# Kernel tuning notes

Hardware: AMD Instinct MI355X
Metric: run time of the kernel (lower is better)

## Reference

```python
import jax, jax.numpy as jnp
import numpy as np

B, T, C = 4, 2048, 768
H = 12  # n_head; head_dim = C // H = 64


def setup_inputs() -> dict:
    key = jax.random.key(0)
    k1, k2, k3, k4, k5 = jax.random.split(key, 5)
    scale = 0.02
    return {
        "x": jax.random.normal(k1, (B, T, C), dtype=jnp.float32),
        "w_attn": jax.random.normal(k2, (C, 3 * C), dtype=jnp.float32) * scale,
        "b_attn": jax.random.normal(k3, (3 * C,), dtype=jnp.float32) * scale,
        "w_proj": jax.random.normal(k4, (C, C), dtype=jnp.float32) * scale,
        "b_proj": jax.random.normal(k5, (C,), dtype=jnp.float32) * scale,
    }


def reference(x, w_attn, b_attn, w_proj, b_proj):
    Bx, Tx, Cx = x.shape
    hd = Cx // H  # head dim
    qkv = x @ w_attn + b_attn                       # [B, T, 3C]
    q, k, v = jnp.split(qkv, 3, axis=2)
    # [B, T, H, hd] -> [B, H, T, hd]
    q = q.reshape(Bx, Tx, H, hd).transpose(0, 2, 1, 3)
    k = k.reshape(Bx, Tx, H, hd).transpose(0, 2, 1, 3)
    v = v.reshape(Bx, Tx, H, hd).transpose(0, 2, 1, 3)
    att = jnp.einsum('bhqd,bhkd->bhqk', q, k) / jnp.sqrt(jnp.float32(hd))
    causal = jnp.tril(jnp.ones((Tx, Tx), dtype=bool))
    att = jnp.where(causal[None, None, :, :], att, -jnp.inf)
    att = jax.nn.softmax(att, axis=-1)
    y = jnp.einsum('bhqk,bhkd->bhqd', att, v)       # [B, H, T, hd]
    y = y.transpose(0, 2, 1, 3).reshape(Bx, Tx, Cx)
    return y @ w_proj + b_proj
```

## Files before the change

kernel.cpp:

```cpp
#include <hip/hip_runtime.h>
#include <hip/hip_bf16.h>

using f32x4 = __attribute__((ext_vector_type(4))) float;
using s16x8 = __attribute__((ext_vector_type(8))) short;

#define MFMA16x16x32(a, b, c) __builtin_amdgcn_mfma_f32_16x16x32_bf16((a), (b), (c), 0, 0, 0)

#define AS_G(p) ((const __attribute__((address_space(1))) void*)(p))
#define AS_L(p) ((__attribute__((address_space(3))) void*)(p))

#define BARRIER_LGKM() do { \
    asm volatile("s_waitcnt lgkmcnt(0)" ::: "memory"); \
    __builtin_amdgcn_s_barrier(); \
} while (0)

static __device__ __forceinline__ unsigned short f2bf(float f) {
    unsigned int u = __float_as_uint(f);
    u = (u + 0x7fffu + ((u >> 16) & 1u)) >> 16;
    return (unsigned short)u;
}
static __device__ __forceinline__ unsigned int cvt_pk_bf2(float lo, float hi) {
    unsigned int r;
    asm("v_cvt_pk_bf16_f32 %0, %1, %2" : "=v"(r) : "v"(lo), "v"(hi));
    return r;
}
static __device__ __forceinline__ int swz128(int r, int c) { return (r * 128 + c) ^ ((r & 7) << 4); }

__global__ __launch_bounds__(256)
void prologue_kernel(const float* __restrict__ x, unsigned short* __restrict__ xb,
                     const float* __restrict__ w_attn, unsigned short* __restrict__ wTa,
                     const float* __restrict__ w_proj, unsigned short* __restrict__ wTp) {
    __shared__ float tile[32][33];
    const int bid = blockIdx.x, tid = threadIdx.x;
    if (bid < 2048) {
        const int n = 8192 * 768;
        int i = (bid * 256 + tid) * 4;
        const int stride = 2048 * 256 * 4;
        for (; i < n; i += stride) {
            float4 v = *(const float4*)(x + i);
            ushort4 o;
            o.x = f2bf(v.x); o.y = f2bf(v.y); o.z = f2bf(v.z); o.w = f2bf(v.w);
            *(ushort4*)(xb + i) = o;
        }
    } else {
        const float* w; unsigned short* wt; int K, N, bx, by;
        if (bid < 3776) {
            int id = bid - 2048; w = w_attn; wt = wTa; K = 768; N = 2304;
            bx = id % 72; by = id / 72;
        } else {
            int id = bid - 3776; w = w_proj; wt = wTp; K = 768; N = 768;
            bx = id % 24; by = id / 24;
        }
        const int tx = tid & 31, ty = tid >> 5;
        const int n0 = bx * 32, k0 = by * 32;
#pragma unroll
        for (int r = 0; r < 4; r++)
            tile[ty * 4 + r][tx] = w[(size_t)(k0 + ty * 4 + r) * N + n0 + tx];
        __syncthreads();
#pragma unroll
        for (int r = 0; r < 4; r++)
            wt[(size_t)(n0 + ty * 4 + r) * K + k0 + tx] = f2bf(tile[tx][ty * 4 + r]);
    }
}

template <bool OUT_BF16>
__global__ __launch_bounds__(256, 2)
void gemm_bt(const unsigned short* __restrict__ A, const unsigned short* __restrict__ Bt,
             const float* __restrict__ bias, void* __restrict__ Cout,
             unsigned short* __restrict__ Vt,
             int M, int N, int K, int ldc, int qcols, float qscale) {
    __shared__ char smem[65536];
    const int tid = threadIdx.x, wid = tid >> 6, lane = tid & 63;
    const int g = lane >> 4, lr = lane & 15;
    const int m0 = blockIdx.y * 128, n0 = blockIdx.x * 128;
    const int wm = wid >> 1, wn = wid & 1;

    f32x4 acc[4][4];
#pragma unroll
    for (int i = 0; i < 4; i++)
#pragma unroll
        for (int j = 0; j < 4; j++) acc[i][j] = f32x4{0.f, 0.f, 0.f, 0.f};

    const int rbase = lane >> 3;
    const int cSw = ((lane & 7) << 4) ^ (rbase << 4);

    auto STAGE = [&](int buf, int kt) {
        char* base = smem + buf * 32768;
#pragma unroll
        for (int ww = 0; ww < 4; ww++) {
            int w = wid * 4 + ww;
            int r = w * 8 + rbase;
            const unsigned short* srcA = A + (size_t)(m0 + r) * K + kt + (cSw >> 1);
            __builtin_amdgcn_global_load_lds(AS_G(srcA), AS_L(base + w * 1024), 16, 0, 0);
            const unsigned short* srcB = Bt + (size_t)(n0 + r) * K + kt + (cSw >> 1);
            __builtin_amdgcn_global_load_lds(AS_G(srcB), AS_L(base + 16384 + w * 1024), 16, 0, 0);
        }
    };

    const int nk = K >> 6;
    STAGE(0, 0);

    for (int t = 0; t < nk; t++) {
        if (t + 1 < nk) {
            STAGE((t + 1) & 1, (t + 1) << 6);
            asm volatile("s_waitcnt vmcnt(8)" ::: "memory");
        } else {
            asm volatile("s_waitcnt vmcnt(0)" ::: "memory");
        }
        __builtin_amdgcn_s_barrier();
        char* cbase = smem + (t & 1) * 32768;
#pragma unroll
        for (int ks = 0; ks < 2; ks++) {
            s16x8 af[4], bfr[4];
#pragma unroll
            for (int i = 0; i < 4; i++)
                af[i] = *(const s16x8*)(cbase + swz128(wm * 64 + i * 16 + lr, ks * 64 + g * 16));
#pragma unroll
            for (int j = 0; j < 4; j++)
                bfr[j] = *(const s16x8*)(cbase + 16384 + swz128(wn * 64 + j * 16 + lr, ks * 64 + g * 16));
#pragma unroll
            for (int i = 0; i < 4; i++)
#pragma unroll
                for (int j = 0; j < 4; j++)
                    acc[i][j] = MFMA16x16x32(af[i], bfr[j], acc[i][j]);
        }
        BARRIER_LGKM();
    }

#pragma unroll
    for (int j = 0; j < 4; j++) {
        int c = n0 + wn * 64 + j * 16 + lr;
        float bv = bias[c];
        float cscale = (c < qcols) ? qscale : 1.0f;
        if (Vt != nullptr && c >= 1536) {
            int h = (c - 1536) >> 6, d = (c - 1536) & 63;
#pragma unroll
            for (int i = 0; i < 4; i++) {
                int r0 = m0 + wm * 64 + i * 16 + g * 4;
                int bb = r0 >> 11, t0 = r0 & 2047;
                ushort4 o4;
                o4.x = f2bf(acc[i][j][0] + bv);
                o4.y = f2bf(acc[i][j][1] + bv);
                o4.z = f2bf(acc[i][j][2] + bv);
                o4.w = f2bf(acc[i][j][3] + bv);
                *(ushort4*)(Vt + ((((size_t)bb * 12 + h) * 64 + d) << 11) + t0) = o4;
            }
        } else {
#pragma unroll
            for (int i = 0; i < 4; i++) {
#pragma unroll
                for (int rg = 0; rg < 4; rg++) {
                    int r = m0 + wm * 64 + i * 16 + g * 4 + rg;
                    float val = (acc[i][j][rg] + bv) * cscale;
                    if constexpr (OUT_BF16)
                        ((unsigned short*)Cout)[(size_t)r * ldc + c] = f2bf(val);
                    else
                        ((float*)Cout)[(size_t)r * ldc + c] = val;
                }
            }
        }
    }
}

__global__ __launch_bounds__(256, 2)
void attn_kernel(const unsigned short* __restrict__ qk, const unsigned short* __restrict__ Vt,
                 unsigned short* __restrict__ y) {
    __shared__ char smem[40960];
    const int tid = threadIdx.x, wid = tid >> 6, lane = tid & 63;
    const int g = lane >> 4, lr = lane & 15;
    const int T = 2048;

    const int s = blockIdx.x;
    const int xcd = s & 7, i = s >> 3;
    const int grp = xcd * 6 + (i >> 4);
    const int qpi = i & 15;
    const int h = grp % 12, b = grp / 12;
    const int qtA = qpi, qtB = 31 - qpi;
    const int q0A = qtA * 64, q0B = qtB * 64;

    const int krow = tid >> 2;
    const int kcol = (tid & 3) * 32;

    const unsigned short* qrowA = qk + (size_t)(b * T + q0A + wid * 16 + lr) * 1536 + h * 64;
    const unsigned short* qrowB = qk + (size_t)(b * T + q0B + wid * 16 + lr) * 1536 + h * 64;
    s16x8 aqA[2], aqB[2];
    aqA[0] = *(const s16x8*)(qrowA + g * 8);
    aqA[1] = *(const s16x8*)(qrowA + 32 + g * 8);
    aqB[0] = *(const s16x8*)(qrowB + g * 8);
    aqB[1] = *(const s16x8*)(qrowB + 32 + g * 8);

    float lA = 0.f, lB = 0.f;
    f32x4 oA[4], oB[4];
#pragma unroll
    for (int r = 0; r < 4; r++) { oA[r] = f32x4{0.f, 0.f, 0.f, 0.f}; oB[r] = f32x4{0.f, 0.f, 0.f, 0.f}; }

    const unsigned short* pkBase = qk + (size_t)(b * T + krow) * 1536 + 768 + h * 64 + (kcol >> 1);
    const unsigned short* pvBase = Vt + ((((size_t)b * 12 + h) * 64 + krow) << 11) + (kcol >> 1);

    const int ntA = qtA + 1, ntB = qtB + 1;

    s16x8 k0 = *(const s16x8*)(pkBase);
    s16x8 k1 = *(const s16x8*)(pkBase + 8);
    s16x8 v0 = *(const s16x8*)(pvBase);
    s16x8 v1 = *(const s16x8*)(pvBase + 8);
    *(s16x8*)(smem + swz128(krow, kcol)) = k0;
    *(s16x8*)(smem + swz128(krow, kcol + 16)) = k1;
    *(s16x8*)(smem + 16384 + swz128(krow, kcol)) = v0;
    *(s16x8*)(smem + 16384 + swz128(krow, kcol + 16)) = v1;
    if (ntB > 1) {
        const unsigned short* pk = pkBase + (size_t)64 * 1536;
        k0 = *(const s16x8*)(pk);
        k1 = *(const s16x8*)(pk + 8);
        const unsigned short* pv = pvBase + 64;
        v0 = *(const s16x8*)(pv);
        v1 = *(const s16x8*)(pv + 8);
    }
    BARRIER_LGKM();

    char* const pbase = smem + 32768 + wid * 2048;
    const int q_rel = wid * 16 + lr;

    for (int t = 0; t < ntB; t++) {
        char* kbase = smem + (t & 1) * 8192;
        char* vbase = smem + 16384 + (t & 1) * 8192;

        {
            f32x4 st[4];
            __builtin_amdgcn_s_setprio(1);
#pragma unroll
            for (int nf = 0; nf < 4; nf++) {
                f32x4 sf = f32x4{0.f, 0.f, 0.f, 0.f};
#pragma unroll
                for (int ks = 0; ks < 2; ks++) {
                    s16x8 ak = *(const s16x8*)(kbase + swz128(nf * 16 + lr, (ks * 32 + g * 8) * 2));
                    sf = MFMA16x16x32(ak, aqB[ks], sf);
                }
                st[nf] = sf;
            }
            __builtin_amdgcn_s_setprio(0);

            const bool diag = (t == ntB - 1);
#pragma unroll
            for (int nf = 0; nf < 4; nf++)
#pragma unroll
                for (int rg = 0; rg < 4; rg++) {
                    float p = exp2f(st[nf][rg]);
                    if (diag && (nf * 16 + g * 4 + rg > q_rel)) p = 0.f;
                    st[nf][rg] = p;
                    lB += p;
                }

#pragma unroll
            for (int nf = 0; nf < 4; nf++) {
                uint2 dw;
                dw.x = cvt_pk_bf2(st[nf][0], st[nf][1]);
                dw.y = cvt_pk_bf2(st[nf][2], st[nf][3]);
                *(uint2*)(pbase + swz128(lr, nf * 32 + g * 8)) = dw;
            }
            s16x8 pf[2];
#pragma unroll
            for (int ks = 0; ks < 2; ks++)
                pf[ks] = *(const s16x8*)(pbase + swz128(lr, ks * 64 + g * 16));

            __builtin_amdgcn_s_setprio(1);
#pragma unroll
            for (int nf = 0; nf < 4; nf++) {
#pragma unroll
                for (int ks = 0; ks < 2; ks++) {
                    s16x8 bv = *(const s16x8*)(vbase + swz128(nf * 16 + lr, ks * 64 + g * 16));
                    oB[nf] = MFMA16x16x32(pf[ks], bv, oB[nf]);
                }
            }
            __builtin_amdgcn_s_setprio(0);
        }

        if (t < ntA) {
            f32x4 st[4];
            __builtin_amdgcn_s_setprio(1);
#pragma unroll
            for (int nf = 0; nf < 4; nf++) {
                f32x4 sf = f32x4{0.f, 0.f, 0.f, 0.f};
#pragma unroll
                for (int ks = 0; ks < 2; ks++) {
                    s16x8 ak = *(const s16x8*)(kbase + swz128(nf * 16 + lr, (ks * 32 + g * 8) * 2));
                    sf = MFMA16x16x32(ak, aqA[ks], sf);
                }
                st[nf] = sf;
            }
            __builtin_amdgcn_s_setprio(0);

            const bool diag = (t == ntA - 1);
#pragma unroll
            for (int nf = 0; nf < 4; nf++)
#pragma unroll
                for (int rg = 0; rg < 4; rg++) {
                    float p = exp2f(st[nf][rg]);
                    if (diag && (nf * 16 + g * 4 + rg > q_rel)) p = 0.f;
                    st[nf][rg] = p;
                    lA += p;
                }

#pragma unroll
            for (int nf = 0; nf < 4; nf++) {
                uint2 dw;
                dw.x = cvt_pk_bf2(st[nf][0], st[nf][1]);
                dw.y = cvt_pk_bf2(st[nf][2], st[nf][3]);
                *(uint2*)(pbase + swz128(lr, nf * 32 + g * 8)) = dw;
            }
            s16x8 pf[2];
#pragma unroll
            for (int ks = 0; ks < 2; ks++)
                pf[ks] = *(const s16x8*)(pbase + swz128(lr, ks * 64 + g * 16));

            __builtin_amdgcn_s_setprio(1);
#pragma unroll
            for (int nf = 0; nf < 4; nf++) {
#pragma unroll
                for (int ks = 0; ks < 2; ks++) {
                    s16x8 bv = *(const s16x8*)(vbase + swz128(nf * 16 + lr, ks * 64 + g * 16));
                    oA[nf] = MFMA16x16x32(pf[ks], bv, oA[nf]);
                }
            }
            __builtin_amdgcn_s_setprio(0);
        }

        if (t + 1 < ntB) {
            char* kn = smem + ((t + 1) & 1) * 8192;
            char* vn = smem + 16384 + ((t + 1) & 1) * 8192;
            *(s16x8*)(kn + swz128(krow, kcol)) = k0;
            *(s16x8*)(kn + swz128(krow, kcol + 16)) = k1;
            *(s16x8*)(vn + swz128(krow, kcol)) = v0;
            *(s16x8*)(vn + swz128(krow, kcol + 16)) = v1;
            if (t + 2 < ntB) {
                const unsigned short* pk = pkBase + (size_t)(t + 2) * 64 * 1536;
                k0 = *(const s16x8*)(pk);
                k1 = *(const s16x8*)(pk + 8);
                const unsigned short* pv = pvBase + (t + 2) * 64;
                v0 = *(const s16x8*)(pv);
                v1 = *(const s16x8*)(pv + 8);
            }
        }
        BARRIER_LGKM();
    }

#pragma unroll
    for (int which = 0; which < 2; which++) {
        float l = which ? lB : lA;
        l += __shfl_xor(l, 16, 64);
        l += __shfl_xor(l, 32, 64);
        float linv = 1.0f / l;
        float linv_q[4];
#pragma unroll
        for (int rg = 0; rg < 4; rg++)
            linv_q[rg] = __shfl(linv, (lane & 48) | (g * 4 + rg), 64);
        const int q0 = which ? q0B : q0A;
        f32x4* o = which ? oB : oA;
#pragma unroll
        for (int nf = 0; nf < 4; nf++) {
#pragma unroll
            for (int rg = 0; rg < 4; rg++) {
                int row = b * T + q0 + wid * 16 + g * 4 + rg;
                int col = h * 64 + nf * 16 + lr;
                y[(size_t)row * 768 + col] = f2bf(o[nf][rg] * linv_q[rg]);
            }
        }
    }
}

extern "C" void kernel_launch(void* const* d_in, const int* in_sizes, int n_in,
                              void* d_out, int out_size, void* d_ws, size_t ws_size,
                              hipStream_t stream) {
    const float* x      = (const float*)d_in[0];
    const float* w_attn = (const float*)d_in[1];
    const float* b_attn = (const float*)d_in[2];
    const float* w_proj = (const float*)d_in[3];
    const float* b_proj = (const float*)d_in[4];

    char* ws = (char*)d_ws;
    unsigned short* qk  = (unsigned short*)(ws);
    unsigned short* Vt  = (unsigned short*)(ws + 25165824);
    unsigned short* wTa = (unsigned short*)(ws + 37748736);
    unsigned short* wTp = (unsigned short*)(ws + 41287680);

    const bool big = ws_size >= (size_t)55050240;
    unsigned short* xb = (unsigned short*)d_out;
    unsigned short* yb = big ? (unsigned short*)(ws + 42467328)
                             : (unsigned short*)((char*)d_out + 12582912);
    float* projOut = big ? (float*)d_out : (float*)ws;

    prologue_kernel<<<4352, 256, 0, stream>>>(x, xb, w_attn, wTa, w_proj, wTp);

    gemm_bt<true><<<dim3(18, 64), 256, 0, stream>>>(xb, wTa, b_attn, (void*)qk, Vt,
                                                    8192, 2304, 768, 1536, 768, 0.1803368801111244f);
    attn_kernel<<<768, 256, 0, stream>>>(qk, Vt, yb);
    gemm_bt<false><<<dim3(6, 64), 256, 0, stream>>>(yb, wTp, b_proj, (void*)projOut, nullptr,
                                                    8192, 768, 768, 768, 0, 1.0f);
    if (!big)
        hipMemcpyAsync(d_out, projOut, 25165824, hipMemcpyDeviceToDevice, stream);
}
```

Baseline: 132.2 us.

## Interleave two query tiles' softmax stages and compute row sums via MFMA

Gives the A and B query tiles separate P buffers in LDS so both score/exp phases run before both PV phases, letting the two independent chains overlap. The per-lane scalar row-sum accumulation and the final shuffles are replaced by MFMAs of P against a vector of bf16 ones. exp2f is swapped for the hardware exp2 builtin. In exchange, LDS use rises to 48 KB, which may affect occupancy, and the row sums are now taken over bf16-rounded P values.

```diff
diff --git a/kernel.cpp b/kernel.cpp
--- a/kernel.cpp
+++ b/kernel.cpp
@@ -165,7 +165,7 @@
 __global__ __launch_bounds__(256, 2)
 void attn_kernel(const unsigned short* __restrict__ qk, const unsigned short* __restrict__ Vt,
                  unsigned short* __restrict__ y) {
-    __shared__ char smem[40960];
+    __shared__ char smem[49152];
     const int tid = threadIdx.x, wid = tid >> 6, lane = tid & 63;
     const int g = lane >> 4, lr = lane & 15;
     const int T = 2048;
@@ -181,6 +181,10 @@
     const int krow = tid >> 2;
     const int kcol = (tid & 3) * 32;
 
+    s16x8 vone;
+#pragma unroll
+    for (int e = 0; e < 8; e++) vone[e] = (short)0x3F80;
+
     const unsigned short* qrowA = qk + (size_t)(b * T + q0A + wid * 16 + lr) * 1536 + h * 64;
     const unsigned short* qrowB = qk + (size_t)(b * T + q0B + wid * 16 + lr) * 1536 + h * 64;
     s16x8 aqA[2], aqB[2];
@@ -189,10 +193,11 @@
     aqB[0] = *(const s16x8*)(qrowB + g * 8);
     aqB[1] = *(const s16x8*)(qrowB + 32 + g * 8);
 
-    float lA = 0.f, lB = 0.f;
-    f32x4 oA[4], oB[4];
+    f32x4 oA[4], oB[4], lsumA, lsumB;
 #pragma unroll
     for (int r = 0; r < 4; r++) { oA[r] = f32x4{0.f, 0.f, 0.f, 0.f}; oB[r] = f32x4{0.f, 0.f, 0.f, 0.f}; }
+    lsumA = f32x4{0.f, 0.f, 0.f, 0.f};
+    lsumB = f32x4{0.f, 0.f, 0.f, 0.f};
 
     const unsigned short* pkBase = qk + (size_t)(b * T + krow) * 1536 + 768 + h * 64 + (kcol >> 1);
     const unsigned short* pvBase = Vt + ((((size_t)b * 12 + h) * 64 + krow) << 11) + (kcol >> 1);
@@ -217,12 +222,14 @@
     }
     BARRIER_LGKM();
 
-    char* const pbase = smem + 32768 + wid * 2048;
+    char* const pbaseB = smem + 32768 + wid * 2048;
+    char* const pbaseA = smem + 40960 + wid * 2048;
     const int q_rel = wid * 16 + lr;
 
     for (int t = 0; t < ntB; t++) {
         char* kbase = smem + (t & 1) * 8192;
         char* vbase = smem + 16384 + (t & 1) * 8192;
+        const bool actA = (t < ntA);
 
         {
             f32x4 st[4];
@@ -238,30 +245,60 @@
                 st[nf] = sf;
             }
             __builtin_amdgcn_s_setprio(0);
-
             const bool diag = (t == ntB - 1);
 #pragma unroll
             for (int nf = 0; nf < 4; nf++)
 #pragma unroll
                 for (int rg = 0; rg < 4; rg++) {
-                    float p = exp2f(st[nf][rg]);
+                    float p = __builtin_amdgcn_exp2f(st[nf][rg]);
                     if (diag && (nf * 16 + g * 4 + rg > q_rel)) p = 0.f;
                     st[nf][rg] = p;
-                    lB += p;
-                }
-
+                }
 #pragma unroll
             for (int nf = 0; nf < 4; nf++) {
                 uint2 dw;
                 dw.x = cvt_pk_bf2(st[nf][0], st[nf][1]);
                 dw.y = cvt_pk_bf2(st[nf][2], st[nf][3]);
-                *(uint2*)(pbase + swz128(lr, nf * 32 + g * 8)) = dw;
-            }
+                *(uint2*)(pbaseB + swz128(lr, nf * 32 + g * 8)) = dw;
+            }
+        }
+        if (actA) {
+            f32x4 st[4];
+            __builtin_amdgcn_s_setprio(1);
+#pragma unroll
+            for (int nf = 0; nf < 4; nf++) {
+                f32x4 sf = f32x4{0.f, 0.f, 0.f, 0.f};
+#pragma unroll
+                for (int ks = 0; ks < 2; ks++) {
+                    s16x8 ak = *(const s16x8*)(kbase + swz128(nf * 16 + lr, (ks * 32 + g * 8) * 2));
+                    sf = MFMA16x16x32(ak, aqA[ks], sf);
+                }
+                st[nf] = sf;
+            }
+            __builtin_amdgcn_s_setprio(0);
+            const bool diag = (t == ntA - 1);
+#pragma unroll
+            for (int nf = 0; nf < 4; nf++)
+#pragma unroll
+                for (int rg = 0; rg < 4; rg++) {
+                    float p = __builtin_amdgcn_exp2f(st[nf][rg]);
+                    if (diag && (nf * 16 + g * 4 + rg > q_rel)) p = 0.f;
+                    st[nf][rg] = p;
+                }
+#pragma unroll
+            for (int nf = 0; nf < 4; nf++) {
+                uint2 dw;
+                dw.x = cvt_pk_bf2(st[nf][0], st[nf][1]);
+                dw.y = cvt_pk_bf2(st[nf][2], st[nf][3]);
+                *(uint2*)(pbaseA + swz128(lr, nf * 32 + g * 8)) = dw;
+            }
+        }
+
+        {
             s16x8 pf[2];
 #pragma unroll
             for (int ks = 0; ks < 2; ks++)
-                pf[ks] = *(const s16x8*)(pbase + swz128(lr, ks * 64 + g * 16));
-
+                pf[ks] = *(const s16x8*)(pbaseB + swz128(lr, ks * 64 + g * 16));
             __builtin_amdgcn_s_setprio(1);
 #pragma unroll
             for (int nf = 0; nf < 4; nf++) {
@@ -271,47 +308,15 @@
                     oB[nf] = MFMA16x16x32(pf[ks], bv, oB[nf]);
                 }
             }
+            lsumB = MFMA16x16x32(pf[0], vone, lsumB);
+            lsumB = MFMA16x16x32(pf[1], vone, lsumB);
             __builtin_amdgcn_s_setprio(0);
         }
-
-        if (t < ntA) {
-            f32x4 st[4];
-            __builtin_amdgcn_s_setprio(1);
-#pragma unroll
-            for (int nf = 0; nf < 4; nf++) {
-                f32x4 sf = f32x4{0.f, 0.f, 0.f, 0.f};
-#pragma unroll
-                for (int ks = 0; ks < 2; ks++) {
-                    s16x8 ak = *(const s16x8*)(kbase + swz128(nf * 16 + lr, (ks * 32 + g * 8) * 2));
-                    sf = MFMA16x16x32(ak, aqA[ks], sf);
-                }
-                st[nf] = sf;
-            }
-            __builtin_amdgcn_s_setprio(0);
-
-            const bool diag = (t == ntA - 1);
-#pragma unroll
-            for (int nf = 0; nf < 4; nf++)
-#pragma unroll
-                for (int rg = 0; rg < 4; rg++) {
-                    float p = exp2f(st[nf][rg]);
-                    if (diag && (nf * 16 + g * 4 + rg > q_rel)) p = 0.f;
-                    st[nf][rg] = p;
-                    lA += p;
-                }
-
-#pragma unroll
-            for (int nf = 0; nf < 4; nf++) {
-                uint2 dw;
-                dw.x = cvt_pk_bf2(st[nf][0], st[nf][1]);
-                dw.y = cvt_pk_bf2(st[nf][2], st[nf][3]);
-                *(uint2*)(pbase + swz128(lr, nf * 32 + g * 8)) = dw;
-            }
+        if (actA) {
             s16x8 pf[2];
 #pragma unroll
             for (int ks = 0; ks < 2; ks++)
-                pf[ks] = *(const s16x8*)(pbase + swz128(lr, ks * 64 + g * 16));
-
+                pf[ks] = *(const s16x8*)(pbaseA + swz128(lr, ks * 64 + g * 16));
             __builtin_amdgcn_s_setprio(1);
 #pragma unroll
             for (int nf = 0; nf < 4; nf++) {
@@ -321,6 +326,8 @@
                     oA[nf] = MFMA16x16x32(pf[ks], bv, oA[nf]);
                 }
             }
+            lsumA = MFMA16x16x32(pf[0], vone, lsumA);
+            lsumA = MFMA16x16x32(pf[1], vone, lsumA);
             __builtin_amdgcn_s_setprio(0);
         }
 
@@ -345,16 +352,12 @@
 
 #pragma unroll
     for (int which = 0; which < 2; which++) {
-        float l = which ? lB : lA;
-        l += __shfl_xor(l, 16, 64);
-        l += __shfl_xor(l, 32, 64);
-        float linv = 1.0f / l;
-        float linv_q[4];
-#pragma unroll
-        for (int rg = 0; rg < 4; rg++)
-            linv_q[rg] = __shfl(linv, (lane & 48) | (g * 4 + rg), 64);
+        const f32x4 lsum = which ? lsumB : lsumA;
         const int q0 = which ? q0B : q0A;
         f32x4* o = which ? oB : oA;
+        float linv_q[4];
+#pragma unroll
+        for (int rg = 0; rg < 4; rg++) linv_q[rg] = 1.0f / lsum[rg];
 #pragma unroll
         for (int nf = 0; nf < 4; nf++) {
 #pragma unroll
```

New measurement: 123.8 us. 6.3% less time.
